# Optimization experiments

Measured on AMD Instinct MI355X. Metric: run time of the kernel, lower is better.

Reference implementation:

```python
import jax, jax.numpy as jnp
import numpy as np

KEEP = 0.9  # eval-mode dropout mask = 1 - dropout, dropout=0.1

def _cell(x, h, c, W, b, H):
    # pre = [h, x] @ W + b ; W: [(H+D), 4H]
    pre = jnp.concatenate([h, x], axis=1) @ W + b
    f, i, o, g = jnp.split(pre, 4, axis=1)
    c1 = jax.nn.sigmoid(f) * c + jax.nn.sigmoid(i) * jnp.tanh(g)
    h1 = jax.nn.sigmoid(o) * jnp.tanh(c1)
    # recurrent dropout in residual form (eval: scalar keep prob)
    h1 = h1 * KEEP + h * (1.0 - KEEP)
    c1 = c1 * KEEP + c * (1.0 - KEEP)
    return h1, c1

def setup_inputs() -> dict:
    key = jax.random.key(0)
    ks = jax.random.split(key, 9)
    B, T, D, H, C = 64, 512, 256, 1024, 128
    s = lambda k, shape, sc: jax.random.normal(k, shape, dtype=jnp.float32) * sc
    return {
        "struct": s(ks[0], (B, T, D), 1.0),
        "W1": s(ks[1], (D + H, 4 * H), 0.02),
        "b1": jnp.zeros((4 * H,), jnp.float32).at[:H].set(1.0),
        "W2": s(ks[2], (H + H, 4 * H), 0.02),
        "b2": jnp.zeros((4 * H,), jnp.float32).at[:H].set(1.0),
        "W3": s(ks[3], (H + H, 4 * H), 0.02),
        "b3": jnp.zeros((4 * H,), jnp.float32).at[:H].set(1.0),
        "fc_w": s(ks[4], (C, H), 0.03),
        "fc_b": jnp.zeros((C,), jnp.float32),
    }

def reference(struct, W1, b1, W2, b2, W3, b3, fc_w, fc_b):
    B, T, D = struct.shape
    H = fc_w.shape[1]
    z = jnp.zeros((B, H), struct.dtype)
    carry0 = (z, z, z, z, z, z)

    def step(carry, x_t):
        h1, c1, h2, c2, h3, c3 = carry
        h1, c1 = _cell(x_t, h1, c1, W1, b1, H)
        h2, c2 = _cell(h1, h2, c2, W2, b2, H)
        h3, c3 = _cell(h2, h3, c3, W3, b3, H)
        return (h1, c1, h2, c2, h3, c3), None

    xs = jnp.swapaxes(struct, 0, 1)  # [T, B, D]
    carry, _ = jax.lax.scan(step, carry0, xs)
    feature = carry[4]  # last-timestep h3, [B, H]
    pred = feature @ fc_w.T + fc_b
    return jax.nn.elu(pred)
```

## Files before the change

### kernel.cpp

```cpp
#include <hip/hip_runtime.h>

typedef _Float16 half8 __attribute__((ext_vector_type(8)));
typedef float f32x4 __attribute__((ext_vector_type(4)));

#define GRIDN 192
#define NTICKS 514
#define TT 512
#define HH 1024

#define MFMA_F16_AB(acc_, a_, b_) \
  asm("v_mfma_f32_16x16x32_f16 %0, %1, %2, %0" : "+v"(acc_) : "v"(a_), "a"(b_))
#define MFMA_F16_AV(acc_, a_, b_) \
  asm("v_mfma_f32_16x16x32_f16 %0, %1, %2, %0" : "+v"(acc_) : "v"(a_), "v"(b_))

#define PIN_AGPR(dst_, src_) asm("" : "=a"(dst_) : "0"(src_))

__device__ __forceinline__ int kfrag(int l, int j) {
  return ((j >> 2) << 4) + (((l >> 4) & 3) << 2) + (j & 3);
}

__device__ __forceinline__ size_t fragoff(int m, int k, int KBv) {
  int rt = m >> 4, mm = m & 15, kb = k >> 5, kk = k & 31;
  int lp = mm | ((kk & 12) << 2);
  int jp = ((kk >> 4) << 2) | (kk & 3);
  return ((size_t)(rt * KBv + kb) * 512) + (size_t)lp * 8 + jp;
}

__device__ __forceinline__ float sigmoidf_(float x) { return 1.0f / (1.0f + __expf(-x)); }
__device__ __forceinline__ float tanhf_(float x)    { return 2.0f / (1.0f + __expf(-2.0f * x)) - 1.0f; }

__global__ __launch_bounds__(256) void pack_b_kernel(const float* __restrict__ W,
                                                     _Float16* __restrict__ dst, int KB) {
  int e = blockIdx.x * 256 + threadIdx.x;
  int total = 64 * KB * 4 * 512;
  if (e >= total) return;
  int j = e & 7, l = (e >> 3) & 63, nt = (e >> 9) & 3;
  int tmp = e >> 11;
  int kb = tmp % KB, cg = tmp / KB;
  int k = kb * 32 + kfrag(l, j);
  int col = nt * 1024 + cg * 16 + (l & 15);
  dst[e] = (_Float16)W[(size_t)k * 4096 + col];
}

__global__ __launch_bounds__(256) void pack_x_kernel(const float* __restrict__ x,
                                                     _Float16* __restrict__ dst) {
  int e = blockIdx.x * 256 + threadIdx.x;
  if (e >= TT * 4 * 8 * 512) return;
  int j = e & 7, l = (e >> 3) & 63;
  int tmp = e >> 9;
  int kb = tmp & 7; tmp >>= 3;
  int rt = tmp & 3; int t = tmp >> 2;
  int b = rt * 16 + (l & 15);
  int d = kb * 32 + kfrag(l, j);
  dst[e] = (_Float16)x[((size_t)b * TT + t) * 256 + d];
}

__device__ __forceinline__ void grid_barrier(unsigned* bar, int tick) {
  asm volatile("s_waitcnt vmcnt(0)" ::: "memory");
  __syncthreads();
  if (threadIdx.x == 0)
    __hip_atomic_fetch_add(&bar[32 * (blockIdx.x & 7)], 1u, __ATOMIC_RELAXED,
                           __HIP_MEMORY_SCOPE_AGENT);
  if (threadIdx.x < 64) {
    const unsigned target = (unsigned)(tick + 1) * 24u;
    for (;;) {
      unsigned v = target;
      if (threadIdx.x < 8)
        v = __hip_atomic_load(&bar[32 * threadIdx.x], __ATOMIC_RELAXED,
                              __HIP_MEMORY_SCOPE_AGENT);
      if (__all(v >= target)) break;
      __builtin_amdgcn_s_sleep(2);
    }
  }
  __syncthreads();
}

template <int CELL, int KBW, int AKB, int UA>
__device__ __forceinline__ void run_cell(float (*red)[16][64][4],
                                         _Float16 (*wlds)[20][512],
                                         const _Float16* __restrict__ Bf,
                                         const _Float16* __restrict__ Ax,
                                         _Float16* Aown, _Float16* Anext,
                                         const float* __restrict__ bias,
                                         float* __restrict__ h3out, unsigned* bar) {
  const int cg   = blockIdx.x & 63;
  const int tid  = threadIdx.x;
  const int warp = tid >> 6;
  const int lane = tid & 63;
  const int KBTOT = (CELL == 0) ? 40 : 64;
  const int kb0   = warp * KBW;

  const int m0    = tid >> 3;
  const int colc0 = (tid & 7) * 2;
  float bv2[2][4];
#pragma unroll
  for (int j = 0; j < 2; ++j)
#pragma unroll
    for (int g = 0; g < 4; ++g) bv2[j][g] = bias[g * HH + cg * 16 + colc0 + j];

  const _Float16* Bbase = Bf + (size_t)cg * KBTOT * 4 * 512 + (size_t)lane * 8;

  if (UA < 4 * KBW) {
#pragma unroll
    for (int u = UA; u < 4 * KBW; ++u) {
      int kk2 = u >> 2, nt2 = u & 3;
      *(half8*)&wlds[warp][u - UA][lane * 8] =
          *(const half8*)(Bbase + ((size_t)(kb0 + kk2) * 4 + nt2) * 512);
    }
  }

  half8 wa[UA];
#pragma unroll
  for (int u = 0; u < UA; ++u) {
    int kk2 = u >> 2, nt2 = u & 3;
    half8 v = *(const half8*)(Bbase + ((size_t)(kb0 + kk2) * 4 + nt2) * 512);
    PIN_AGPR(wa[u], v);
  }

  float cs[2][2] = {{0.f, 0.f}, {0.f, 0.f}};
  float hs[2][2] = {{0.f, 0.f}, {0.f, 0.f}};

  for (int tick = 0; tick < NTICKS; ++tick) {
    const int t = tick - CELL;
    if (t >= 0 && t < TT) {
      const int wpar = tick & 1, rpar = wpar ^ 1;
      const _Float16* Ard = Aown + (size_t)rpar * 4 * AKB * 512 + (size_t)lane * 8;
      const _Float16* Axt = Ax + (size_t)t * 4 * 8 * 512 + (size_t)lane * 8;

      auto aptr = [&](int kk, int rt) -> const _Float16* {
        int kb = kb0 + kk;
        if (CELL == 0 && kb >= 32) return Axt + ((size_t)rt * 8 + (kb - 32)) * 512;
        return Ard + ((size_t)rt * AKB + kb) * 512;
      };

      half8 av[8][4];
      f32x4 acc[4][4];
#pragma unroll
      for (int a = 0; a < 4; ++a)
#pragma unroll
        for (int b2 = 0; b2 < 4; ++b2) acc[a][b2] = (f32x4){0.f, 0.f, 0.f, 0.f};

#define ISSUE4(kk)                                                    \
  {                                                                   \
    _Pragma("unroll") for (int rt = 0; rt < 4; ++rt)                  \
        asm volatile("global_load_dwordx4 %0, %1, off sc0 sc1"        \
                     : "=v"(av[(kk) & 7][rt])                         \
                     : "v"(aptr((kk), rt)));                          \
  }

#define STEP(kk)                                                               \
  if constexpr ((kk) < KBW) {                                                  \
    if constexpr ((kk) + 7 < KBW) ISSUE4((kk) + 7);                            \
    asm volatile("s_waitcnt vmcnt(%0)" ::                                      \
                     "n"((kk) + 7 < KBW ? 28 : (KBW - 1 - (kk)) * 4)           \
                 : "memory");                                                  \
    __builtin_amdgcn_sched_barrier(0);                                         \
    _Pragma("unroll") for (int nt = 0; nt < 4; ++nt) {                         \
      const int u = (kk)*4 + nt;                                               \
      if (u < UA) {                                                            \
        _Pragma("unroll") for (int rt = 0; rt < 4; ++rt)                       \
            MFMA_F16_AB(acc[rt][nt], av[(kk) & 7][rt], wa[u < UA ? u : 0]);    \
      } else {                                                                 \
        half8 bw =                                                             \
            *(const half8*)&wlds[warp][(u >= UA ? u - UA : 0)][lane * 8];      \
        _Pragma("unroll") for (int rt = 0; rt < 4; ++rt)                       \
            MFMA_F16_AV(acc[rt][nt], av[(kk) & 7][rt], bw);                    \
      }                                                                        \
    }                                                                          \
  }

      ISSUE4(0); ISSUE4(1); ISSUE4(2); ISSUE4(3); ISSUE4(4); ISSUE4(5); ISSUE4(6);
      STEP(0)  STEP(1)  STEP(2)  STEP(3)  STEP(4)  STEP(5)  STEP(6)  STEP(7)
      STEP(8)  STEP(9)  STEP(10) STEP(11) STEP(12) STEP(13) STEP(14) STEP(15)
#undef ISSUE4
#undef STEP

      asm volatile("s_nop 7\n\ts_nop 7");

#pragma unroll
      for (int rt = 0; rt < 4; ++rt)
#pragma unroll
        for (int nt = 0; nt < 4; ++nt)
          *(f32x4*)&red[warp][rt * 4 + nt][lane][0] = acc[rt][nt];
      __syncthreads();

#pragma unroll
      for (int e = 0; e < 2; ++e) {
        const int m = m0 + e * 32;
        const int rt4 = (m >> 4) * 4, lc_hi = ((m & 15) >> 2) << 4, rr = m & 3;
        float hnf[2];
        union { _Float16 h[2]; unsigned u; } pk;
#pragma unroll
        for (int j = 0; j < 2; ++j) {
          const int lc = (colc0 + j) | lc_hi;
          float pre[4];
#pragma unroll
          for (int g = 0; g < 4; ++g)
            pre[g] = red[0][rt4 + g][lc][rr] + red[1][rt4 + g][lc][rr] +
                     red[2][rt4 + g][lc][rr] + red[3][rt4 + g][lc][rr] + bv2[j][g];
          float sf = sigmoidf_(pre[0]), si = sigmoidf_(pre[1]), so = sigmoidf_(pre[2]);
          float tg = tanhf_(pre[3]);
          float c_old = cs[e][j], h_old = hs[e][j];
          float c0 = sf * c_old + si * tg;
          float h0 = so * tanhf_(c0);
          float cn = 0.9f * c0 + 0.1f * c_old;
          float hn = 0.9f * h0 + 0.1f * h_old;
          cs[e][j] = cn;
          hs[e][j] = hn;
          hnf[j] = hn;
          pk.h[j] = (_Float16)hn;
        }
        const int hcol0 = cg * 16 + colc0;
        {
          size_t off = (size_t)wpar * 4 * AKB * 512 + fragoff(m, hcol0, AKB);
          __hip_atomic_store((unsigned*)(Aown + off), pk.u, __ATOMIC_RELAXED,
                             __HIP_MEMORY_SCOPE_AGENT);
        }
        if (CELL < 2) {
          size_t off = (size_t)wpar * 4 * 64 * 512 + fragoff(m, 1024 + hcol0, 64);
          __hip_atomic_store((unsigned*)(Anext + off), pk.u, __ATOMIC_RELAXED,
                             __HIP_MEMORY_SCOPE_AGENT);
        }
        if (CELL == 2 && t == TT - 1) {
          h3out[m * HH + hcol0]     = hnf[0];
          h3out[m * HH + hcol0 + 1] = hnf[1];
        }
      }
    }

    if (tick < NTICKS - 1) grid_barrier(bar, tick);
  }
}

__global__ __launch_bounds__(256, 1) void lstm_coop(
    const _Float16* __restrict__ Bf1, const _Float16* __restrict__ Bf2,
    const _Float16* __restrict__ Bf3, const _Float16* __restrict__ Ax,
    _Float16* A1h, _Float16* A2v, _Float16* A3v, float* h3,
    const float* __restrict__ bb1, const float* __restrict__ bb2, const float* __restrict__ bb3,
    unsigned* bar) {
  __shared__ float red[4][16][64][4];
  __shared__ _Float16 wlds[4][20][512];
  const int cell = blockIdx.x >> 6;
  if (cell == 0)
    run_cell<0, 10, 32, 40>(red, wlds, Bf1, Ax, A1h, A2v, bb1, nullptr, bar);
  else if (cell == 1)
    run_cell<1, 16, 64, 44>(red, wlds, Bf2, Ax, A2v, A3v, bb2, nullptr, bar);
  else
    run_cell<2, 16, 64, 44>(red, wlds, Bf3, Ax, A3v, nullptr, bb3, h3, bar);
}

__global__ __launch_bounds__(256) void fc_kernel(const float* __restrict__ h3,
                                                 const float* __restrict__ fcw,
                                                 const float* __restrict__ fcb,
                                                 float* __restrict__ out) {
  int wid = (blockIdx.x * 256 + threadIdx.x) >> 6;
  int lane = threadIdx.x & 63;
  if (wid >= 64 * 128) return;
  int b = wid >> 7, cc = wid & 127;
  float s = 0.f;
#pragma unroll
  for (int i = 0; i < 16; ++i) {
    int k = i * 64 + lane;
    s += h3[b * HH + k] * fcw[cc * HH + k];
  }
#pragma unroll
  for (int o = 32; o; o >>= 1) s += __shfl_xor(s, o, 64);
  if (lane == 0) {
    s += fcb[cc];
    out[b * 128 + cc] = s > 0.f ? s : (__expf(s) - 1.0f);
  }
}

extern "C" void kernel_launch(void* const* d_in, const int* in_sizes, int n_in,
                              void* d_out, int out_size, void* d_ws, size_t ws_size,
                              hipStream_t stream) {
  const float* xs  = (const float*)d_in[0];
  const float* W1  = (const float*)d_in[1];
  const float* b1  = (const float*)d_in[2];
  const float* W2  = (const float*)d_in[3];
  const float* b2  = (const float*)d_in[4];
  const float* W3  = (const float*)d_in[5];
  const float* b3  = (const float*)d_in[6];
  const float* fcw = (const float*)d_in[7];
  const float* fcb = (const float*)d_in[8];
  float* out = (float*)d_out;

  char* p = (char*)d_ws;
  auto alloc = [&](size_t bytes) {
    char* r = p;
    p += (bytes + 255) & ~(size_t)255;
    return r;
  };

  char* zbase = p;
  _Float16* A1h = (_Float16*)alloc((size_t)2 * 4 * 32 * 512 * 2);
  _Float16* A2v = (_Float16*)alloc((size_t)2 * 4 * 64 * 512 * 2);
  _Float16* A3v = (_Float16*)alloc((size_t)2 * 4 * 64 * 512 * 2);
  unsigned* bar = (unsigned*)alloc(1024);
  size_t zbytes = (size_t)(p - zbase);

  float* h3 = (float*)alloc((size_t)64 * 1024 * 4);
  _Float16* Bf1 = (_Float16*)alloc((size_t)64 * 40 * 4 * 512 * 2);
  _Float16* Bf2 = (_Float16*)alloc((size_t)64 * 64 * 4 * 512 * 2);
  _Float16* Bf3 = (_Float16*)alloc((size_t)64 * 64 * 4 * 512 * 2);
  _Float16* Axp = (_Float16*)alloc((size_t)TT * 4 * 8 * 512 * 2);

  (void)hipMemsetAsync(zbase, 0, zbytes, stream);

  {
    int tot1 = 64 * 40 * 4 * 512, tot23 = 64 * 64 * 4 * 512;
    pack_b_kernel<<<(tot1 + 255) / 256, 256, 0, stream>>>(W1, Bf1, 40);
    pack_b_kernel<<<(tot23 + 255) / 256, 256, 0, stream>>>(W2, Bf2, 64);
    pack_b_kernel<<<(tot23 + 255) / 256, 256, 0, stream>>>(W3, Bf3, 64);
    int totx = TT * 4 * 8 * 512;
    pack_x_kernel<<<(totx + 255) / 256, 256, 0, stream>>>(xs, Axp);
  }

  lstm_coop<<<GRIDN, 256, 0, stream>>>(Bf1, Bf2, Bf3, Axp, A1h, A2v, A3v, h3,
                                       b1, b2, b3, bar);

  fc_kernel<<<(64 * 128 * 64 + 255) / 256, 256, 0, stream>>>(h3, fcw, fcb, out);
}
```

Before: 3.893 ms.

## Stage recurrent state into per-XCD buffers so A loads hit local L2

Adds 64 helper blocks, bringing the grid to 256. Each tick, every block copies a slice of the shared hidden-state buffers into a staging copy owned by its XCD, then waits on a per-XCD counter. The GEMM A-operand loads then read the XCD-local copy with sc0 only instead of the system-coherent sc0 sc1, which is meant to cut cross-XCD coherent traffic. The cost is an extra copy phase and a per-XCD sync every tick. The staging copy is written with plain stores and read with sc0 only, so it depends on L2 coherence within one XCD, and the grid barrier now waits on more blocks.

```diff
diff --git a/kernel.cpp b/kernel.cpp
--- a/kernel.cpp
+++ b/kernel.cpp
@@ -3,10 +3,13 @@
 typedef _Float16 half8 __attribute__((ext_vector_type(8)));
 typedef float f32x4 __attribute__((ext_vector_type(4)));
 
-#define GRIDN 192
+#define GRIDN 256
 #define NTICKS 514
 #define TT 512
 #define HH 1024
+
+#define SLOT_E 327680u
+#define XCD_E  (2u * SLOT_E)
 
 #define MFMA_F16_AB(acc_, a_, b_) \
   asm("v_mfma_f32_16x16x32_f16 %0, %1, %2, %0" : "+v"(acc_) : "v"(a_), "a"(b_))
@@ -14,6 +17,12 @@
   asm("v_mfma_f32_16x16x32_f16 %0, %1, %2, %0" : "+v"(acc_) : "v"(a_), "v"(b_))
 
 #define PIN_AGPR(dst_, src_) asm("" : "=a"(dst_) : "0"(src_))
+
+__device__ __forceinline__ int get_xcd() {
+  int x;
+  asm("s_getreg_b32 %0, hwreg(HW_REG_XCC_ID)" : "=s"(x));
+  return x & 7;
+}
 
 __device__ __forceinline__ int kfrag(int l, int j) {
   return ((j >> 2) << 4) + (((l >> 4) & 3) << 2) + (j & 3);
@@ -62,7 +71,7 @@
     __hip_atomic_fetch_add(&bar[32 * (blockIdx.x & 7)], 1u, __ATOMIC_RELAXED,
                            __HIP_MEMORY_SCOPE_AGENT);
   if (threadIdx.x < 64) {
-    const unsigned target = (unsigned)(tick + 1) * 24u;
+    const unsigned target = (unsigned)(tick + 1) * 32u;
     for (;;) {
       unsigned v = target;
       if (threadIdx.x < 8)
@@ -75,20 +84,72 @@
   __syncthreads();
 }
 
+__device__ __forceinline__ void copy_phase(const _Float16* A1, const _Float16* A2,
+                                           const _Float16* A3, _Float16* stg,
+                                           int rank, int xcd, int rpar, int tid,
+                                           unsigned* stagectr) {
+  const int c0 = rank * 5;
+  if (c0 + 4 < 160) {
+    half8 v0, v1, v2, v3, v4;
+    auto srcp = [&](int c) -> const _Float16* {
+      if (c < 32) return A1 + (size_t)rpar * 65536 + (size_t)c * 2048 + tid * 8;
+      if (c < 96) return A2 + (size_t)rpar * 131072 + (size_t)(c - 32) * 2048 + tid * 8;
+      return A3 + (size_t)rpar * 131072 + (size_t)(c - 96) * 2048 + tid * 8;
+    };
+    _Float16* dst = stg + (size_t)xcd * XCD_E + (size_t)rpar * SLOT_E +
+                    (size_t)c0 * 2048 + tid * 8;
+#define CPLD(vv, cc) \
+  asm volatile("global_load_dwordx4 %0, %1, off sc0 sc1" : "=v"(vv) : "v"(srcp(cc)))
+    CPLD(v0, c0); CPLD(v1, c0 + 1); CPLD(v2, c0 + 2); CPLD(v3, c0 + 3); CPLD(v4, c0 + 4);
+#undef CPLD
+    asm volatile("s_waitcnt vmcnt(4)" ::: "memory");
+    *(half8*)(dst + 0 * 2048) = v0;
+    asm volatile("s_waitcnt vmcnt(4)" ::: "memory");
+    *(half8*)(dst + 1 * 2048) = v1;
+    asm volatile("s_waitcnt vmcnt(4)" ::: "memory");
+    *(half8*)(dst + 2 * 2048) = v2;
+    asm volatile("s_waitcnt vmcnt(4)" ::: "memory");
+    *(half8*)(dst + 3 * 2048) = v3;
+    asm volatile("s_waitcnt vmcnt(4)" ::: "memory");
+    *(half8*)(dst + 4 * 2048) = v4;
+  }
+  asm volatile("s_waitcnt vmcnt(0)" ::: "memory");
+  __syncthreads();
+  if (tid == 0)
+    __hip_atomic_fetch_add(&stagectr[32 * xcd], 1u, __ATOMIC_RELAXED,
+                           __HIP_MEMORY_SCOPE_AGENT);
+}
+
+__device__ __forceinline__ void run_helper(const _Float16* A1, const _Float16* A2,
+                                           const _Float16* A3, _Float16* stg,
+                                           unsigned* stagectr, unsigned* bar,
+                                           int xcd, int rank) {
+  for (int tick = 0; tick < NTICKS; ++tick) {
+    copy_phase(A1, A2, A3, stg, rank, xcd, (tick & 1) ^ 1, threadIdx.x, stagectr);
+    if (tick < NTICKS - 1) grid_barrier(bar, tick);
+  }
+}
+
 template <int CELL, int KBW, int AKB, int UA>
 __device__ __forceinline__ void run_cell(float (*red)[16][64][4],
                                          _Float16 (*wlds)[20][512],
                                          const _Float16* __restrict__ Bf,
                                          const _Float16* __restrict__ Ax,
-                                         _Float16* Aown, _Float16* Anext,
+                                         const _Float16* A1, const _Float16* A2,
+                                         const _Float16* A3, _Float16* stg,
                                          const float* __restrict__ bias,
-                                         float* __restrict__ h3out, unsigned* bar) {
+                                         float* __restrict__ h3out, unsigned* bar,
+                                         unsigned* stagectr, int xcd, int rank) {
   const int cg   = blockIdx.x & 63;
   const int tid  = threadIdx.x;
   const int warp = tid >> 6;
   const int lane = tid & 63;
   const int KBTOT = (CELL == 0) ? 40 : 64;
   const int kb0   = warp * KBW;
+  const unsigned POFF = (CELL == 0) ? 0u : (CELL == 1) ? 65536u : 196608u;
+
+  _Float16* Aown = (CELL == 0) ? (_Float16*)A1 : (CELL == 1) ? (_Float16*)A2 : (_Float16*)A3;
+  _Float16* Anext = (CELL == 0) ? (_Float16*)A2 : (CELL == 1) ? (_Float16*)A3 : nullptr;
 
   const int m0    = tid >> 3;
   const int colc0 = (tid & 7) * 2;
@@ -121,16 +182,27 @@
   float hs[2][2] = {{0.f, 0.f}, {0.f, 0.f}};
 
   for (int tick = 0; tick < NTICKS; ++tick) {
+    const int wpar = tick & 1, rpar = wpar ^ 1;
+
+    copy_phase(A1, A2, A3, stg, rank, xcd, rpar, tid, stagectr);
+    if (tid == 0) {
+      const unsigned tgt = 32u * (unsigned)(tick + 1);
+      while (__hip_atomic_load(&stagectr[32 * xcd], __ATOMIC_RELAXED,
+                               __HIP_MEMORY_SCOPE_AGENT) < tgt)
+        __builtin_amdgcn_s_sleep(1);
+    }
+    __syncthreads();
+
     const int t = tick - CELL;
     if (t >= 0 && t < TT) {
-      const int wpar = tick & 1, rpar = wpar ^ 1;
-      const _Float16* Ard = Aown + (size_t)rpar * 4 * AKB * 512 + (size_t)lane * 8;
+      const _Float16* As = stg + (size_t)xcd * XCD_E + (size_t)rpar * SLOT_E + POFF +
+                           (size_t)lane * 8;
       const _Float16* Axt = Ax + (size_t)t * 4 * 8 * 512 + (size_t)lane * 8;
 
       auto aptr = [&](int kk, int rt) -> const _Float16* {
         int kb = kb0 + kk;
         if (CELL == 0 && kb >= 32) return Axt + ((size_t)rt * 8 + (kb - 32)) * 512;
-        return Ard + ((size_t)rt * AKB + kb) * 512;
+        return As + ((size_t)rt * AKB + kb) * 512;
       };
 
       half8 av[8][4];
@@ -143,7 +215,7 @@
 #define ISSUE4(kk)                                                    \
   {                                                                   \
     _Pragma("unroll") for (int rt = 0; rt < 4; ++rt)                  \
-        asm volatile("global_load_dwordx4 %0, %1, off sc0 sc1"        \
+        asm volatile("global_load_dwordx4 %0, %1, off sc0"            \
                      : "=v"(av[(kk) & 7][rt])                         \
                      : "v"(aptr((kk), rt)));                          \
   }
@@ -235,18 +307,33 @@
 __global__ __launch_bounds__(256, 1) void lstm_coop(
     const _Float16* __restrict__ Bf1, const _Float16* __restrict__ Bf2,
     const _Float16* __restrict__ Bf3, const _Float16* __restrict__ Ax,
-    _Float16* A1h, _Float16* A2v, _Float16* A3v, float* h3,
+    _Float16* A1h, _Float16* A2v, _Float16* A3v, _Float16* stg, float* h3,
     const float* __restrict__ bb1, const float* __restrict__ bb2, const float* __restrict__ bb3,
-    unsigned* bar) {
+    unsigned* bar, unsigned* xcdcnt, unsigned* stagectr) {
   __shared__ float red[4][16][64][4];
   __shared__ _Float16 wlds[4][20][512];
+  __shared__ int sh_xcd, sh_rank;
+  if (threadIdx.x == 0) {
+    int x = get_xcd();
+    sh_xcd = x;
+    sh_rank = (int)__hip_atomic_fetch_add(&xcdcnt[32 * x], 1u, __ATOMIC_RELAXED,
+                                          __HIP_MEMORY_SCOPE_AGENT);
+  }
+  __syncthreads();
+  const int xcd = sh_xcd, rank = sh_rank;
+
   const int cell = blockIdx.x >> 6;
   if (cell == 0)
-    run_cell<0, 10, 32, 40>(red, wlds, Bf1, Ax, A1h, A2v, bb1, nullptr, bar);
+    run_cell<0, 10, 32, 40>(red, wlds, Bf1, Ax, A1h, A2v, A3v, stg, bb1, nullptr, bar,
+                            stagectr, xcd, rank);
   else if (cell == 1)
-    run_cell<1, 16, 64, 44>(red, wlds, Bf2, Ax, A2v, A3v, bb2, nullptr, bar);
+    run_cell<1, 16, 64, 44>(red, wlds, Bf2, Ax, A1h, A2v, A3v, stg, bb2, nullptr, bar,
+                            stagectr, xcd, rank);
+  else if (cell == 2)
+    run_cell<2, 16, 64, 44>(red, wlds, Bf3, Ax, A1h, A2v, A3v, stg, bb3, h3, bar,
+                            stagectr, xcd, rank);
   else
-    run_cell<2, 16, 64, 44>(red, wlds, Bf3, Ax, A3v, nullptr, bb3, h3, bar);
+    run_helper(A1h, A2v, A3v, stg, stagectr, bar, xcd, rank);
 }
 
 __global__ __launch_bounds__(256) void fc_kernel(const float* __restrict__ h3,
@@ -296,7 +383,9 @@
   _Float16* A1h = (_Float16*)alloc((size_t)2 * 4 * 32 * 512 * 2);
   _Float16* A2v = (_Float16*)alloc((size_t)2 * 4 * 64 * 512 * 2);
   _Float16* A3v = (_Float16*)alloc((size_t)2 * 4 * 64 * 512 * 2);
-  unsigned* bar = (unsigned*)alloc(1024);
+  unsigned* bar      = (unsigned*)alloc(1024);
+  unsigned* xcdcnt   = (unsigned*)alloc(1024);
+  unsigned* stagectr = (unsigned*)alloc(1024);
   size_t zbytes = (size_t)(p - zbase);
 
   float* h3 = (float*)alloc((size_t)64 * 1024 * 4);
@@ -304,6 +393,7 @@
   _Float16* Bf2 = (_Float16*)alloc((size_t)64 * 64 * 4 * 512 * 2);
   _Float16* Bf3 = (_Float16*)alloc((size_t)64 * 64 * 4 * 512 * 2);
   _Float16* Axp = (_Float16*)alloc((size_t)TT * 4 * 8 * 512 * 2);
+  _Float16* stg = (_Float16*)alloc((size_t)8 * XCD_E * 2);
 
   (void)hipMemsetAsync(zbase, 0, zbytes, stream);
 
@@ -316,8 +406,8 @@
     pack_x_kernel<<<(totx + 255) / 256, 256, 0, stream>>>(xs, Axp);
   }
 
-  lstm_coop<<<GRIDN, 256, 0, stream>>>(Bf1, Bf2, Bf3, Axp, A1h, A2v, A3v, h3,
-                                       b1, b2, b3, bar);
+  lstm_coop<<<GRIDN, 256, 0, stream>>>(Bf1, Bf2, Bf3, Axp, A1h, A2v, A3v, stg, h3,
+                                       b1, b2, b3, bar, xcdcnt, stagectr);
 
   fc_kernel<<<(64 * 128 * 64 + 255) / 256, 256, 0, stream>>>(h3, fcw, fcb, out);
 }
```

New measurement: 6.139 ms. 1.58x slower.
